# Optimization experiments

Hardware: AMD Instinct MI355X
Metric: run time of the kernel (lower is better)

Reference implementation:

```python
import jax, jax.numpy as jnp
import numpy as np

N_HEADS = 16
D_EMBED = 1024


def setup_inputs() -> dict:
    key = jax.random.key(0)
    k_x, k_win, k_bin, k_wout, k_bout = jax.random.split(key, 5)
    B, S, D = 4, 2048, D_EMBED
    # weights stored as (in, out) so y = x @ W + b (equivalent to torch Linear)
    x = jax.random.normal(k_x, (B, S, D), dtype=jnp.float32)
    W_in = jax.random.normal(k_win, (D, 3 * D), dtype=jnp.float32) * (D ** -0.5)
    b_in = jax.random.normal(k_bin, (3 * D,), dtype=jnp.float32) * 0.02
    W_out = jax.random.normal(k_wout, (D, D), dtype=jnp.float32) * (D ** -0.5)
    b_out = jax.random.normal(k_bout, (D,), dtype=jnp.float32) * 0.02
    return {"x": x, "W_in": W_in, "b_in": b_in, "W_out": W_out, "b_out": b_out,
            "causal_mask": 1}


def reference(x, W_in, b_in, W_out, b_out, causal_mask):
    B, S, D = x.shape
    H = N_HEADS
    dh = D // H
    qkv = x @ W_in + b_in                      # [B,S,3D]
    q, k, v = jnp.split(qkv, 3, axis=-1)
    q = q.reshape(B, S, H, dh)
    k = k.reshape(B, S, H, dh)
    v = v.reshape(B, S, H, dh)
    scores = jnp.einsum('bqhd,bkhd->bhqk', q, k)   # [B,H,S,S]
    if causal_mask:
        # original masks with -inf BEFORE scaling; -inf/sqrt(dh) == -inf
        tri = jnp.triu(jnp.ones((S, S), dtype=bool), k=1)
        scores = jnp.where(tri, -jnp.inf, scores)
    scores = scores / jnp.sqrt(jnp.asarray(dh, dtype=scores.dtype))
    attn = jax.nn.softmax(scores, axis=-1)
    out = jnp.einsum('bhqk,bkhd->bqhd', attn, v).reshape(B, S, D)
    return out @ W_out + b_out
```

## Files before the change

### kernel.cpp

```cpp
#include <hip/hip_runtime.h>
#include <hip/hip_bf16.h>
#include <stdint.h>
#include <string.h>

#define S_LEN 2048
#define NH    16
#define DH    64
#define D_EMB 1024
#define CSCALE 0.18033688011112042f

typedef __attribute__((ext_vector_type(8)))  short short8;
typedef __attribute__((ext_vector_type(4)))  float f32x4;
typedef __attribute__((ext_vector_type(16))) float f32x16;
typedef __attribute__((ext_vector_type(4)))  uint32_t u32x4;

__device__ __forceinline__ unsigned short f2bf(float f) {
  uint32_t u = __builtin_bit_cast(uint32_t, f);
  uint32_t r = (u + 0x7FFFu + ((u >> 16) & 1u)) >> 16;
  return (unsigned short)r;
}

__device__ __forceinline__ uint32_t pkbf(float a, float b) {
  float2 f; f.x = a; f.y = b;
  __hip_bfloat162 h = __float22bfloat162_rn(f);
  uint32_t r;
  memcpy(&r, &h, 4);
  return r;
}

__device__ __forceinline__ uint32_t pktr(float a, float b) {
  return __builtin_amdgcn_perm(__builtin_bit_cast(uint32_t, b),
                               __builtin_bit_cast(uint32_t, a), 0x07060302u);
}

__device__ __forceinline__ float fexp2(float x) {
#if __has_builtin(__builtin_amdgcn_exp2f)
  return __builtin_amdgcn_exp2f(x);
#else
  float r;
  asm("v_exp_f32 %0, %1\ns_nop 0" : "=v"(r) : "v"(x));
  return r;
#endif
}

__device__ __forceinline__ void gload16(const void* g, void* l) {
  __builtin_amdgcn_global_load_lds(
      (__attribute__((address_space(1))) void*)(g),
      (__attribute__((address_space(3))) void*)(l),
      16, 0, 0);
}

__device__ __forceinline__ f32x16 mfma32(short8 a, short8 b, f32x16 c) {
  return __builtin_amdgcn_mfma_f32_32x32x16_bf16(a, b, c, 0, 0, 0);
}


__global__ __launch_bounds__(256)
void cvt_bf16(const float* __restrict__ in, unsigned short* __restrict__ out, int n) {
  int i = (blockIdx.x * 256 + threadIdx.x) * 4;
  if (i >= n) return;
  float4 v = *(const float4*)&in[i];
  ushort4 o;
  o.x = f2bf(v.x); o.y = f2bf(v.y); o.z = f2bf(v.z); o.w = f2bf(v.w);
  *(ushort4*)&out[i] = o;
}

__global__ __launch_bounds__(256)
void transpose_cvt(const float* __restrict__ in, unsigned short* __restrict__ out,
                   int R, int C) {
  __shared__ float t[64][65];
  const int nbr = R >> 6;
  const int br = (blockIdx.x % nbr) << 6;
  const int bc = (blockIdx.x / nbr) << 6;
  const int tid = threadIdx.x;
  const int tr = tid >> 4;
  const int tc = (tid & 15) << 2;
#pragma unroll
  for (int i = 0; i < 4; ++i) {
    float4 v = *(const float4*)&in[(size_t)(br + tr + i * 16) * C + bc + tc];
    t[tr + i * 16][tc + 0] = v.x;
    t[tr + i * 16][tc + 1] = v.y;
    t[tr + i * 16][tc + 2] = v.z;
    t[tr + i * 16][tc + 3] = v.w;
  }
  __syncthreads();
#pragma unroll
  for (int i = 0; i < 4; ++i) {
    int c = tr + i * 16;
    ushort4 o;
    o.x = f2bf(t[tc + 0][c]);
    o.y = f2bf(t[tc + 1][c]);
    o.z = f2bf(t[tc + 2][c]);
    o.w = f2bf(t[tc + 3][c]);
    *(ushort4*)&out[(size_t)(bc + c) * R + br + tc] = o;
  }
}


template <int MODE>
__global__ __launch_bounds__(256, 2)
void gemm_bt(const unsigned short* __restrict__ A,
             const unsigned short* __restrict__ Bt,
             const float* __restrict__ bias,
             unsigned short* __restrict__ q_out,
             unsigned short* __restrict__ k_out,
             unsigned short* __restrict__ v_out,
             float* __restrict__ f_out,
             int M, int N, int K) {
  __shared__ __attribute__((aligned(16))) unsigned short As[2][128 * 64];
  __shared__ __attribute__((aligned(16))) unsigned short Bs[2][128 * 64];
  const int tid  = threadIdx.x;
  const int lane = tid & 63;
  const int w    = tid >> 6;
  const int grp  = lane >> 4;
  const int lc   = lane & 15;
  const int nbn  = N >> 7;
  const int bm   = blockIdx.x / nbn;
  const int bn   = blockIdx.x % nbn;
  const int wr   = w >> 1, wc = w & 1;

  f32x4 acc[4][4];
#pragma unroll
  for (int m = 0; m < 4; ++m)
#pragma unroll
    for (int n = 0; n < 4; ++n) acc[m][n] = f32x4{0.f, 0.f, 0.f, 0.f};

  const int srow = lane >> 3;
  const int scol = ((lane & 7) ^ srow) * 8;
  const int nkt  = K >> 6;

#define GSTAGE(buf_, kt_) do {                                               \
    _Pragma("unroll")                                                        \
    for (int c_ = 0; c_ < 4; ++c_) {                                         \
      const int rc_ = w * 32 + c_ * 8;                                       \
      gload16(&A[(size_t)(bm * 128 + rc_ + srow) * K + (kt_) * 64 + scol],   \
              (void*)(&As[buf_][rc_ * 64]));                                 \
      gload16(&Bt[(size_t)(bn * 128 + rc_ + srow) * K + (kt_) * 64 + scol],  \
              (void*)(&Bs[buf_][rc_ * 64]));                                 \
    }                                                                        \
  } while (0)

  GSTAGE(0, 0);
  __syncthreads();

  for (int kt = 0; kt < nkt; ++kt) {
    const int cur = kt & 1;
    if (kt + 1 < nkt) GSTAGE(cur ^ 1, kt + 1);
#pragma unroll
    for (int kk = 0; kk < 2; ++kk) {
      short8 af[4], bf[4];
#pragma unroll
      for (int m = 0; m < 4; ++m) {
        const int row = wr * 64 + m * 16 + lc;
        const int cb  = ((kk * 4 + grp) ^ (lc & 7)) * 8;
        af[m] = *(const short8*)(&As[cur][row * 64 + cb]);
      }
#pragma unroll
      for (int n = 0; n < 4; ++n) {
        const int row = wc * 64 + n * 16 + lc;
        const int cb  = ((kk * 4 + grp) ^ (lc & 7)) * 8;
        bf[n] = *(const short8*)(&Bs[cur][row * 64 + cb]);
      }
      __builtin_amdgcn_s_setprio(1);
#pragma unroll
      for (int m = 0; m < 4; ++m)
#pragma unroll
        for (int n = 0; n < 4; ++n)
          acc[m][n] = __builtin_amdgcn_mfma_f32_16x16x32_bf16(af[m], bf[n], acc[m][n], 0, 0, 0);
      __builtin_amdgcn_s_setprio(0);
    }
    __syncthreads();
  }
#undef GSTAGE

  const int gm0 = bm * 128 + wr * 64;
  const int gn0 = bn * 128 + wc * 64;
  if (MODE == 0) {
    const int seg = gn0 >> 10;
#pragma unroll
    for (int m = 0; m < 4; ++m) {
#pragma unroll
      for (int n = 0; n < 4; ++n) {
        const int gn = gn0 + n * 16 + lc;
        const float bv = bias[gn];
        const int j = gn & 1023;
        const int h = j >> 6, d = j & 63;
        const int gmb = gm0 + m * 16 + grp * 4;
        const int b = gmb >> 11;
        const size_t bhb = ((size_t)(b * NH + h) * 32 + ((gmb & 2047) >> 6)) * 4096;
        if (seg == 2) {
          const size_t vi = bhb + ((d >> 5) * 4 + m) * 512 +
                            ((d & 31) + (grp >> 1) * 32) * 8 + (grp & 1) * 4;
          uint2 dv;
          dv.x = pkbf(acc[m][n][0] + bv, acc[m][n][1] + bv);
          dv.y = pkbf(acc[m][n][2] + bv, acc[m][n][3] + bv);
          *(uint2*)&v_out[vi] = dv;
        } else {
#pragma unroll
          for (int r = 0; r < 4; ++r) {
            const int s = (gmb + r) & 2047;
            float v = acc[m][n][r] + bv;
            if (seg == 0) v *= CSCALE;
            const size_t idx = bhb + (((s >> 5) & 1) * 4 + (d >> 4)) * 512 +
                               ((s & 31) + ((d >> 3) & 1) * 32) * 8 + (d & 7);
            if (seg == 0) q_out[idx] = f2bf(v); else k_out[idx] = f2bf(v);
          }
        }
      }
    }
  } else {
#pragma unroll
    for (int m = 0; m < 4; ++m) {
#pragma unroll
      for (int n = 0; n < 4; ++n) {
        const int gn = gn0 + n * 16 + lc;
        const float bv = bias[gn];
#pragma unroll
        for (int r = 0; r < 4; ++r) {
          const int gm = gm0 + m * 16 + grp * 4 + r;
          f_out[(size_t)gm * N + gn] = acc[m][n][r] + bv;
        }
      }
    }
  }
}


__global__ __launch_bounds__(256, 3)
void attn_fwd9(const unsigned short* __restrict__ Qp,
               const unsigned short* __restrict__ Kp,
               const unsigned short* __restrict__ Vp,
               unsigned short* __restrict__ Aout) {
  __shared__ __attribute__((aligned(16))) unsigned short Ks[2][4096];
  __shared__ __attribute__((aligned(16))) unsigned short Vs[2][4096];
  const int tid  = threadIdx.x;
  const int lane = tid & 63, w = tid >> 6;
  const int q32  = lane & 31;
  const int hi   = lane >> 5;
  const int lof  = lane * 8;
  const int g    = blockIdx.x;
  const int t    = 15 - (g >> 6);
  const int bh   = (((g >> 3) & 7) << 3) | (g & 7);
  const int b    = bh >> 4, h = bh & 15;
  const size_t fb = (size_t)bh * 32;

#define STAGE(bf_, kb_) do {                                          \
    const size_t sb_ = (fb + (size_t)(kb_)) * 4096 + tid * 8;         \
    gload16(Kp + sb_,        (void*)&Ks[bf_][tid * 8]);               \
    gload16(Kp + sb_ + 2048, (void*)&Ks[bf_][2048 + tid * 8]);        \
    gload16(Vp + sb_,        (void*)&Vs[bf_][tid * 8]);               \
    gload16(Vp + sb_ + 2048, (void*)&Vs[bf_][2048 + tid * 8]);        \
  } while (0)

  const int qw0 = t * 128 + w * 32;
  const int qkb = 2 * t + (w >> 1), qsub = w & 1;

  short8 qf[4];
#pragma unroll
  for (int s = 0; s < 4; ++s)
    qf[s] = *(const short8*)(Qp + (fb + qkb) * 4096 + (qsub * 4 + s) * 512 + lof);

  f32x16 oa, ob;
#pragma unroll
  for (int rr = 0; rr < 16; ++rr) { oa[rr] = 0.f; ob[rr] = 0.f; }
  float l = 0.f;

  const int nbt = 2 * t + 2;
  STAGE(0, 0);
  asm volatile("s_waitcnt vmcnt(0)" ::: "memory");
  __syncthreads();
  int buf = 0;

#pragma unroll 1
  for (int kb = 0; kb < nbt; ++kb) {
    if (kb + 1 < nbt) STAGE(buf ^ 1, kb + 1);
    const int kvb = kb << 6;
    if (kvb <= qw0 + 31) {
      const unsigned short* kl = &Ks[buf][0];
      const unsigned short* vl = &Vs[buf][0];

      f32x16 c0, c1;
#pragma unroll
      for (int rr = 0; rr < 16; ++rr) { c0[rr] = 0.f; c1[rr] = -1e30f; }
      const bool do1 = (kvb + 32 <= qw0 + 31);
      __builtin_amdgcn_s_setprio(1);
#pragma unroll
      for (int s = 0; s < 4; ++s) {
        short8 kf = *(const short8*)(kl + s * 512 + lof);
        c0 = mfma32(kf, qf[s], c0);
      }
      if (do1) {
#pragma unroll
        for (int rr = 0; rr < 16; ++rr) c1[rr] = 0.f;
#pragma unroll
        for (int s = 0; s < 4; ++s) {
          short8 kf = *(const short8*)(kl + (4 + s) * 512 + lof);
          c1 = mfma32(kf, qf[s], c1);
        }
      }
      __builtin_amdgcn_s_setprio(0);

      if (kvb + 63 > qw0) {
        const int thr = qw0 + q32 - kvb;
#pragma unroll
        for (int rr = 0; rr < 16; ++rr) {
          const int k0 = (rr & 3) + 8 * (rr >> 2) + 4 * hi;
          if (k0 > thr)      c0[rr] = -1e30f;
          if (k0 + 32 > thr) c1[rr] = -1e30f;
        }
      }

#pragma unroll
      for (int rr = 0; rr < 16; ++rr) c0[rr] = fexp2(c0[rr]);
#pragma unroll
      for (int rr = 0; rr < 16; ++rr) c1[rr] = fexp2(c1[rr]);
      float tp[8];
#pragma unroll
      for (int i = 0; i < 8; ++i)
        tp[i] = (c0[i] + c0[i + 8]) + (c1[i] + c1[i + 8]);
      l += ((tp[0] + tp[1]) + (tp[2] + tp[3])) +
           ((tp[4] + tp[5]) + (tp[6] + tp[7]));

#pragma unroll
      for (int ks = 0; ks < 4; ++ks) {
        if (ks >= 2 && !do1) break;
        uint32_t pA, pB, pC, pD;
        if (ks == 0) {
          pA = pktr(c0[0],  c0[1]);  pB = pktr(c0[2],  c0[3]);
          pC = pktr(c0[4],  c0[5]);  pD = pktr(c0[6],  c0[7]);
        } else if (ks == 1) {
          pA = pktr(c0[8],  c0[9]);  pB = pktr(c0[10], c0[11]);
          pC = pktr(c0[12], c0[13]); pD = pktr(c0[14], c0[15]);
        } else if (ks == 2) {
          pA = pktr(c1[0],  c1[1]);  pB = pktr(c1[2],  c1[3]);
          pC = pktr(c1[4],  c1[5]);  pD = pktr(c1[6],  c1[7]);
        } else {
          pA = pktr(c1[8],  c1[9]);  pB = pktr(c1[10], c1[11]);
          pC = pktr(c1[12], c1[13]); pD = pktr(c1[14], c1[15]);
        }
        auto r0 = __builtin_amdgcn_permlane32_swap(pA, pC, false, false);
        auto r1 = __builtin_amdgcn_permlane32_swap(pB, pD, false, false);
        u32x4 fw; fw[0] = r0[0]; fw[1] = r1[0]; fw[2] = r0[1]; fw[3] = r1[1];
        const short8 frag = __builtin_bit_cast(short8, fw);
        oa = mfma32(*(const short8*)(vl + ks * 512 + lof), frag, oa);
        ob = mfma32(*(const short8*)(vl + (4 + ks) * 512 + lof), frag, ob);
      }
    }
    asm volatile("s_waitcnt vmcnt(0)" ::: "memory");
    __syncthreads();
    buf ^= 1;
  }

  l += __shfl_xor(l, 32);
  const float inv = 1.0f / l;
  unsigned short* ebuf = (unsigned short*)Ks;
  unsigned short* prow = ebuf + (w * 32 + q32) * 64;
  const int swz = (q32 & 7) << 3;
#pragma unroll
  for (int gg = 0; gg < 4; ++gg) {
    const int d0 = 8 * gg + 4 * hi;
    uint2 da, db;
    da.x = pkbf(oa[4 * gg] * inv,     oa[4 * gg + 1] * inv);
    da.y = pkbf(oa[4 * gg + 2] * inv, oa[4 * gg + 3] * inv);
    db.x = pkbf(ob[4 * gg] * inv,     ob[4 * gg + 1] * inv);
    db.y = pkbf(ob[4 * gg + 2] * inv, ob[4 * gg + 3] * inv);
    *(uint2*)&prow[d0 ^ swz]        = da;
    *(uint2*)&prow[(d0 + 32) ^ swz] = db;
  }
  asm volatile("s_waitcnt lgkmcnt(0)" ::: "memory");
  __builtin_amdgcn_sched_barrier(0);
  const int er = lane >> 1, eh = lane & 1;
  const int rswz = (er & 7) << 3;
  const unsigned short* lr = ebuf + (w * 32 + er) * 64;
  unsigned short* op = Aout + ((size_t)(b * S_LEN + qw0 + er)) * D_EMB + h * DH + eh * 32;
#pragma unroll
  for (int jj = 0; jj < 4; ++jj) {
    short8 ov = *(const short8*)&lr[(eh * 32 + jj * 8) ^ rswz];
    *(short8*)(op + jj * 8) = ov;
  }
#undef STAGE
}


extern "C" void kernel_launch(void* const* d_in, const int* in_sizes, int n_in,
                              void* d_out, int out_size, void* d_ws, size_t ws_size,
                              hipStream_t stream) {
  const float* x     = (const float*)d_in[0];
  const float* W_in  = (const float*)d_in[1];
  const float* b_in  = (const float*)d_in[2];
  const float* W_out = (const float*)d_in[3];
  const float* b_out = (const float*)d_in[4];

  char* ws = (char*)d_ws;
  unsigned short* xb  = (unsigned short*)(ws);
  unsigned short* Wti = (unsigned short*)(ws + 16777216);
  unsigned short* Wto = (unsigned short*)(ws + 23068672);
  unsigned short* Qb  = (unsigned short*)(ws + 25165824);
  unsigned short* Kb  = (unsigned short*)(ws + 41943040);
  unsigned short* Vb  = (unsigned short*)(ws + 58720256);
  float* out = (float*)d_out;

  cvt_bf16<<<8192, 256, 0, stream>>>(x, xb, 8388608);
  transpose_cvt<<<16 * 48, 256, 0, stream>>>(W_in, Wti, 1024, 3072);
  transpose_cvt<<<16 * 16, 256, 0, stream>>>(W_out, Wto, 1024, 1024);

  gemm_bt<0><<<64 * 24, 256, 0, stream>>>(xb, Wti, b_in, Qb, Kb, Vb, nullptr,
                                          8192, 3072, 1024);
  attn_fwd9<<<1024, 256, 0, stream>>>(Qb, Kb, Vb, xb);
  gemm_bt<1><<<64 * 8, 256, 0, stream>>>(xb, Wto, b_out, nullptr, nullptr, nullptr, out,
                                         8192, 1024, 1024);
}
```

Measured before the change: 160.3 us.

## Replace GEMM with 8-wave 256-row tiles and split A/B prefetch scheduling

Replaces the 128x128 four-wave GEMM with an eight-wave kernel using 256-row tiles (256 or 128 columns), raising per-block data reuse. It stages A and B loads at different points in the loop, uses explicit waitcnt/barrier sequencing, and loads A fragments in two halves to cap register pressure. The larger tile produces fewer blocks: 384 for the QKV projection and 256 for the output projection, which may underfill the GPU's compute units and lower occupancy. The hand-written vmcnt counts depend on how many loads are in flight, so they are fragile.

```diff
diff --git a/kernel.cpp b/kernel.cpp
--- a/kernel.cpp
+++ b/kernel.cpp
@@ -52,6 +52,9 @@
 
 __device__ __forceinline__ f32x16 mfma32(short8 a, short8 b, f32x16 c) {
   return __builtin_amdgcn_mfma_f32_32x32x16_bf16(a, b, c, 0, 0, 0);
+}
+__device__ __forceinline__ f32x4 mfma16(short8 a, short8 b, f32x4 c) {
+  return __builtin_amdgcn_mfma_f32_16x16x32_bf16(a, b, c, 0, 0, 0);
 }
 
 
@@ -97,109 +100,152 @@
 }
 
 
-template <int MODE>
-__global__ __launch_bounds__(256, 2)
-void gemm_bt(const unsigned short* __restrict__ A,
-             const unsigned short* __restrict__ Bt,
-             const float* __restrict__ bias,
-             unsigned short* __restrict__ q_out,
-             unsigned short* __restrict__ k_out,
-             unsigned short* __restrict__ v_out,
-             float* __restrict__ f_out,
-             int M, int N, int K) {
-  __shared__ __attribute__((aligned(16))) unsigned short As[2][128 * 64];
-  __shared__ __attribute__((aligned(16))) unsigned short Bs[2][128 * 64];
+template <int MODE, int BN>
+__global__ __launch_bounds__(512, 2)
+void gemm8(const unsigned short* __restrict__ A,
+           const unsigned short* __restrict__ Bt,
+           const float* __restrict__ bias,
+           unsigned short* __restrict__ q_out,
+           unsigned short* __restrict__ k_out,
+           unsigned short* __restrict__ v_out,
+           float* __restrict__ f_out,
+           int M, int N, int K) {
+  constexpr int NF = BN / 64;
+  constexpr int BL = BN / 64;
+  __shared__ __attribute__((aligned(16))) unsigned short As[2][256 * 64];
+  __shared__ __attribute__((aligned(16))) unsigned short Bs[2][BN * 64];
   const int tid  = threadIdx.x;
   const int lane = tid & 63;
+  const int grp  = lane >> 4, lc = lane & 15;
   const int w    = tid >> 6;
-  const int grp  = lane >> 4;
-  const int lc   = lane & 15;
-  const int nbn  = N >> 7;
+  const int wr   = w >> 2, wc = w & 3;
+  const int nbn  = N / BN;
   const int bm   = blockIdx.x / nbn;
   const int bn   = blockIdx.x % nbn;
-  const int wr   = w >> 1, wc = w & 1;
-
-  f32x4 acc[4][4];
-#pragma unroll
-  for (int m = 0; m < 4; ++m)
-#pragma unroll
-    for (int n = 0; n < 4; ++n) acc[m][n] = f32x4{0.f, 0.f, 0.f, 0.f};
-
-  const int srow = lane >> 3;
-  const int scol = ((lane & 7) ^ srow) * 8;
   const int nkt  = K >> 6;
 
-#define GSTAGE(buf_, kt_) do {                                               \
-    _Pragma("unroll")                                                        \
-    for (int c_ = 0; c_ < 4; ++c_) {                                         \
-      const int rc_ = w * 32 + c_ * 8;                                       \
-      gload16(&A[(size_t)(bm * 128 + rc_ + srow) * K + (kt_) * 64 + scol],   \
-              (void*)(&As[buf_][rc_ * 64]));                                 \
-      gload16(&Bt[(size_t)(bn * 128 + rc_ + srow) * K + (kt_) * 64 + scol],  \
-              (void*)(&Bs[buf_][rc_ * 64]));                                 \
-    }                                                                        \
+  f32x4 acc[8][NF];
+#pragma unroll
+  for (int mf = 0; mf < 8; ++mf)
+#pragma unroll
+    for (int nf = 0; nf < NF; ++nf) acc[mf][nf] = f32x4{0.f, 0.f, 0.f, 0.f};
+
+#define GSA(slot_, kt_) do {                                                  \
+    _Pragma("unroll")                                                         \
+    for (int j_ = 0; j_ < 4; ++j_) {                                          \
+      const int c_ = j_ * 512 + tid;                                          \
+      const int r_ = c_ >> 3, s_ = c_ & 7;                                    \
+      gload16(&A[(size_t)(bm * 256 + r_) * K + (kt_) * 64 +                   \
+                 ((s_ ^ (r_ & 7)) << 3)],                                     \
+              (void*)(&As[slot_][c_ << 3]));                                  \
+    }                                                                         \
   } while (0)
-
-  GSTAGE(0, 0);
-  __syncthreads();
+#define GSB(slot_, kt_) do {                                                  \
+    _Pragma("unroll")                                                         \
+    for (int j_ = 0; j_ < BL; ++j_) {                                         \
+      const int c_ = j_ * 512 + tid;                                          \
+      const int r_ = c_ >> 3, s_ = c_ & 7;                                    \
+      gload16(&Bt[(size_t)(bn * BN + r_) * K + (kt_) * 64 +                   \
+                  ((s_ ^ (r_ & 7)) << 3)],                                    \
+              (void*)(&Bs[slot_][c_ << 3]));                                  \
+    }                                                                         \
+  } while (0)
+
+  GSA(0, 0);
+  GSB(0, 0);
 
   for (int kt = 0; kt < nkt; ++kt) {
-    const int cur = kt & 1;
-    if (kt + 1 < nkt) GSTAGE(cur ^ 1, kt + 1);
-#pragma unroll
-    for (int kk = 0; kk < 2; ++kk) {
-      short8 af[4], bf[4];
-#pragma unroll
-      for (int m = 0; m < 4; ++m) {
-        const int row = wr * 64 + m * 16 + lc;
-        const int cb  = ((kk * 4 + grp) ^ (lc & 7)) * 8;
-        af[m] = *(const short8*)(&As[cur][row * 64 + cb]);
-      }
-#pragma unroll
-      for (int n = 0; n < 4; ++n) {
-        const int row = wc * 64 + n * 16 + lc;
-        const int cb  = ((kk * 4 + grp) ^ (lc & 7)) * 8;
-        bf[n] = *(const short8*)(&Bs[cur][row * 64 + cb]);
-      }
-      __builtin_amdgcn_s_setprio(1);
-#pragma unroll
-      for (int m = 0; m < 4; ++m)
-#pragma unroll
-        for (int n = 0; n < 4; ++n)
-          acc[m][n] = __builtin_amdgcn_mfma_f32_16x16x32_bf16(af[m], bf[n], acc[m][n], 0, 0, 0);
-      __builtin_amdgcn_s_setprio(0);
+    const int slot = kt & 1;
+    asm volatile("s_waitcnt lgkmcnt(0)" ::: "memory");
+    __builtin_amdgcn_sched_barrier(0);
+    __builtin_amdgcn_s_barrier();
+    __builtin_amdgcn_sched_barrier(0);
+    if (kt + 1 < nkt) {
+      GSA(slot ^ 1, kt + 1);
+      asm volatile("s_waitcnt vmcnt(4)" ::: "memory");
+    } else {
+      asm volatile("s_waitcnt vmcnt(0)" ::: "memory");
     }
-    __syncthreads();
-  }
-#undef GSTAGE
-
-  const int gm0 = bm * 128 + wr * 64;
-  const int gn0 = bn * 128 + wc * 64;
+    __builtin_amdgcn_sched_barrier(0);
+    __builtin_amdgcn_s_barrier();
+    __builtin_amdgcn_sched_barrier(0);
+
+    short8 bf[NF][2];
+#pragma unroll
+    for (int nf = 0; nf < NF; ++nf)
+#pragma unroll
+      for (int kk = 0; kk < 2; ++kk) {
+        const int br = wc * (BN / 4) + nf * 16 + lc;
+        bf[nf][kk] = *(const short8*)(&Bs[slot][br * 64 +
+                        (((kk * 4 + grp) ^ (lc & 7)) << 3)]);
+      }
+    short8 af[4][2];
+#pragma unroll
+    for (int mf = 0; mf < 4; ++mf)
+#pragma unroll
+      for (int kk = 0; kk < 2; ++kk) {
+        const int ar = wr * 128 + mf * 16 + lc;
+        af[mf][kk] = *(const short8*)(&As[slot][ar * 64 +
+                        (((kk * 4 + grp) ^ (lc & 7)) << 3)]);
+      }
+    if (kt + 1 < nkt) GSB(slot ^ 1, kt + 1);
+    __builtin_amdgcn_s_setprio(1);
+#pragma unroll
+    for (int mf = 0; mf < 4; ++mf)
+#pragma unroll
+      for (int nf = 0; nf < NF; ++nf) {
+        acc[mf][nf] = mfma16(af[mf][0], bf[nf][0], acc[mf][nf]);
+        acc[mf][nf] = mfma16(af[mf][1], bf[nf][1], acc[mf][nf]);
+      }
+    __builtin_amdgcn_s_setprio(0);
+#pragma unroll
+    for (int mf = 0; mf < 4; ++mf)
+#pragma unroll
+      for (int kk = 0; kk < 2; ++kk) {
+        const int ar = wr * 128 + (mf + 4) * 16 + lc;
+        af[mf][kk] = *(const short8*)(&As[slot][ar * 64 +
+                        (((kk * 4 + grp) ^ (lc & 7)) << 3)]);
+      }
+    __builtin_amdgcn_s_setprio(1);
+#pragma unroll
+    for (int mf = 0; mf < 4; ++mf)
+#pragma unroll
+      for (int nf = 0; nf < NF; ++nf) {
+        acc[mf + 4][nf] = mfma16(af[mf][0], bf[nf][0], acc[mf + 4][nf]);
+        acc[mf + 4][nf] = mfma16(af[mf][1], bf[nf][1], acc[mf + 4][nf]);
+      }
+    __builtin_amdgcn_s_setprio(0);
+  }
+#undef GSA
+#undef GSB
+
+  const int gm0w = bm * 256 + wr * 128;
+  const int gn0w = bn * BN + wc * (BN / 4);
   if (MODE == 0) {
-    const int seg = gn0 >> 10;
-#pragma unroll
-    for (int m = 0; m < 4; ++m) {
-#pragma unroll
-      for (int n = 0; n < 4; ++n) {
-        const int gn = gn0 + n * 16 + lc;
+    const int seg = gn0w >> 10;
+#pragma unroll
+    for (int mf = 0; mf < 8; ++mf) {
+#pragma unroll
+      for (int nf = 0; nf < NF; ++nf) {
+        const int gn = gn0w + nf * 16 + lc;
         const float bv = bias[gn];
-        const int j = gn & 1023;
-        const int h = j >> 6, d = j & 63;
-        const int gmb = gm0 + m * 16 + grp * 4;
+        const int jj = gn & 1023;
+        const int h = jj >> 6, d = jj & 63;
+        const int gmb = gm0w + mf * 16 + grp * 4;
         const int b = gmb >> 11;
         const size_t bhb = ((size_t)(b * NH + h) * 32 + ((gmb & 2047) >> 6)) * 4096;
         if (seg == 2) {
-          const size_t vi = bhb + ((d >> 5) * 4 + m) * 512 +
+          const size_t vi = bhb + ((d >> 5) * 4 + (mf & 3)) * 512 +
                             ((d & 31) + (grp >> 1) * 32) * 8 + (grp & 1) * 4;
           uint2 dv;
-          dv.x = pkbf(acc[m][n][0] + bv, acc[m][n][1] + bv);
-          dv.y = pkbf(acc[m][n][2] + bv, acc[m][n][3] + bv);
+          dv.x = pkbf(acc[mf][nf][0] + bv, acc[mf][nf][1] + bv);
+          dv.y = pkbf(acc[mf][nf][2] + bv, acc[mf][nf][3] + bv);
           *(uint2*)&v_out[vi] = dv;
         } else {
 #pragma unroll
           for (int r = 0; r < 4; ++r) {
             const int s = (gmb + r) & 2047;
-            float v = acc[m][n][r] + bv;
+            float v = acc[mf][nf][r] + bv;
             if (seg == 0) v *= CSCALE;
             const size_t idx = bhb + (((s >> 5) & 1) * 4 + (d >> 4)) * 512 +
                                ((s & 31) + ((d >> 3) & 1) * 32) * 8 + (d & 7);
@@ -210,15 +256,15 @@
     }
   } else {
 #pragma unroll
-    for (int m = 0; m < 4; ++m) {
-#pragma unroll
-      for (int n = 0; n < 4; ++n) {
-        const int gn = gn0 + n * 16 + lc;
+    for (int mf = 0; mf < 8; ++mf) {
+#pragma unroll
+      for (int nf = 0; nf < NF; ++nf) {
+        const int gn = gn0w + nf * 16 + lc;
         const float bv = bias[gn];
 #pragma unroll
         for (int r = 0; r < 4; ++r) {
-          const int gm = gm0 + m * 16 + grp * 4 + r;
-          f_out[(size_t)gm * N + gn] = acc[m][n][r] + bv;
+          const int gm = gm0w + mf * 16 + grp * 4 + r;
+          f_out[(size_t)gm * N + gn] = acc[mf][nf][r] + bv;
         }
       }
     }
@@ -404,9 +450,9 @@
   transpose_cvt<<<16 * 48, 256, 0, stream>>>(W_in, Wti, 1024, 3072);
   transpose_cvt<<<16 * 16, 256, 0, stream>>>(W_out, Wto, 1024, 1024);
 
-  gemm_bt<0><<<64 * 24, 256, 0, stream>>>(xb, Wti, b_in, Qb, Kb, Vb, nullptr,
-                                          8192, 3072, 1024);
+  gemm8<0, 256><<<32 * 12, 512, 0, stream>>>(xb, Wti, b_in, Qb, Kb, Vb, nullptr,
+                                             8192, 3072, 1024);
   attn_fwd9<<<1024, 256, 0, stream>>>(Qb, Kb, Vb, xb);
-  gemm_bt<1><<<64 * 8, 256, 0, stream>>>(xb, Wto, b_out, nullptr, nullptr, nullptr, out,
-                                         8192, 1024, 1024);
-}
+  gemm8<1, 128><<<32 * 8, 512, 0, stream>>>(xb, Wto, b_out, nullptr, nullptr, nullptr, out,
+                                            8192, 1024, 1024);
+}
```

Result: slower. 174.8 us (+9.1%).

## Replace double-buffered GEMM staging with single buffer to raise occupancy

Applied to the files above, without the earlier changes.

Drops the double-buffered LDS tiles in the bf16 GEMM and loads each k-tile into a single buffer, with a barrier before compute. This halves LDS use per block (64KB to 32KB) and raises the launch-bound occupancy hint from 2 to 3 blocks per CU. The aim is to hide load latency through more resident waves rather than through software prefetch, at the cost of no load/compute overlap within a block.

```diff
diff --git a/kernel.cpp b/kernel.cpp
--- a/kernel.cpp
+++ b/kernel.cpp
@@ -98,7 +98,7 @@
 
 
 template <int MODE>
-__global__ __launch_bounds__(256, 2)
+__global__ __launch_bounds__(256, 3)
 void gemm_bt(const unsigned short* __restrict__ A,
              const unsigned short* __restrict__ Bt,
              const float* __restrict__ bias,
@@ -107,8 +107,8 @@
              unsigned short* __restrict__ v_out,
              float* __restrict__ f_out,
              int M, int N, int K) {
-  __shared__ __attribute__((aligned(16))) unsigned short As[2][128 * 64];
-  __shared__ __attribute__((aligned(16))) unsigned short Bs[2][128 * 64];
+  __shared__ __attribute__((aligned(16))) unsigned short As[128 * 64];
+  __shared__ __attribute__((aligned(16))) unsigned short Bs[128 * 64];
   const int tid  = threadIdx.x;
   const int lane = tid & 63;
   const int w    = tid >> 6;
@@ -129,23 +129,16 @@
   const int scol = ((lane & 7) ^ srow) * 8;
   const int nkt  = K >> 6;
 
-#define GSTAGE(buf_, kt_) do {                                               \
-    _Pragma("unroll")                                                        \
-    for (int c_ = 0; c_ < 4; ++c_) {                                         \
-      const int rc_ = w * 32 + c_ * 8;                                       \
-      gload16(&A[(size_t)(bm * 128 + rc_ + srow) * K + (kt_) * 64 + scol],   \
-              (void*)(&As[buf_][rc_ * 64]));                                 \
-      gload16(&Bt[(size_t)(bn * 128 + rc_ + srow) * K + (kt_) * 64 + scol],  \
-              (void*)(&Bs[buf_][rc_ * 64]));                                 \
-    }                                                                        \
-  } while (0)
-
-  GSTAGE(0, 0);
-  __syncthreads();
-
   for (int kt = 0; kt < nkt; ++kt) {
-    const int cur = kt & 1;
-    if (kt + 1 < nkt) GSTAGE(cur ^ 1, kt + 1);
+#pragma unroll
+    for (int c = 0; c < 4; ++c) {
+      const int rc = w * 32 + c * 8;
+      gload16(&A[(size_t)(bm * 128 + rc + srow) * K + kt * 64 + scol],
+              (void*)(&As[rc * 64]));
+      gload16(&Bt[(size_t)(bn * 128 + rc + srow) * K + kt * 64 + scol],
+              (void*)(&Bs[rc * 64]));
+    }
+    __syncthreads();
 #pragma unroll
     for (int kk = 0; kk < 2; ++kk) {
       short8 af[4], bf[4];
@@ -153,13 +146,13 @@
       for (int m = 0; m < 4; ++m) {
         const int row = wr * 64 + m * 16 + lc;
         const int cb  = ((kk * 4 + grp) ^ (lc & 7)) * 8;
-        af[m] = *(const short8*)(&As[cur][row * 64 + cb]);
+        af[m] = *(const short8*)(&As[row * 64 + cb]);
       }
 #pragma unroll
       for (int n = 0; n < 4; ++n) {
         const int row = wc * 64 + n * 16 + lc;
         const int cb  = ((kk * 4 + grp) ^ (lc & 7)) * 8;
-        bf[n] = *(const short8*)(&Bs[cur][row * 64 + cb]);
+        bf[n] = *(const short8*)(&Bs[row * 64 + cb]);
       }
       __builtin_amdgcn_s_setprio(1);
 #pragma unroll
@@ -171,7 +164,6 @@
     }
     __syncthreads();
   }
-#undef GSTAGE
 
   const int gm0 = bm * 128 + wr * 64;
   const int gn0 = bn * 128 + wc * 64;
```

Measured after the change: 152.9 us. 4.6% less time.
